# Performance work log

Hardware: AMD Instinct MI355X
Metric: run time of the kernel (lower is better)

The kernel has to match this reference:

```python
import jax, jax.numpy as jnp
import numpy as np

N = 100000   # nodes
E = 1600000  # edges
F_IN = 32    # num_features
H = 16       # hidden_size (hardcoded as conv2 input in source)
C = 10       # num_classes
K = 2        # kernel_size (dim=1)


def setup_inputs() -> dict:
    key = jax.random.key(0)
    ks = jax.random.split(key, 9)
    x = jax.random.normal(ks[0], (N, F_IN), dtype=jnp.float32)
    edge_index = jax.random.randint(ks[1], (2, E), 0, N, dtype=jnp.int64)
    edge_attr = jax.random.uniform(ks[2], (E, 1), dtype=jnp.float32)
    s1 = 1.0 / np.sqrt(F_IN)
    s2 = 1.0 / np.sqrt(H)
    W1 = jax.random.normal(ks[3], (K, F_IN, H), dtype=jnp.float32) * s1
    root1 = jax.random.normal(ks[4], (F_IN, H), dtype=jnp.float32) * s1
    b1 = jnp.zeros((H,), dtype=jnp.float32)
    W2 = jax.random.normal(ks[5], (K, H, C), dtype=jnp.float32) * s2
    root2 = jax.random.normal(ks[6], (H, C), dtype=jnp.float32) * s2
    b2 = jnp.zeros((C,), dtype=jnp.float32)
    return {"x": x, "edge_index": edge_index, "edge_attr": edge_attr,
            "W1": W1, "root1": root1, "b1": b1,
            "W2": W2, "root2": root2, "b2": b2}


def spline_conv(x, edge_index, edge_attr, W, root, bias, num_nodes):
    # Open B-spline, degree 1: hat-function basis over K knots.
    k = W.shape[0]
    src, dst = edge_index[0], edge_index[1]
    v = edge_attr[:, 0] * (k - 1)                                   # [E]
    grid = jnp.arange(k, dtype=v.dtype)
    basis = jnp.maximum(0.0, 1.0 - jnp.abs(v[:, None] - grid[None, :]))  # [E,K]
    xe = x[src]                                                      # [E,in] gather
    msg = jnp.einsum('ei,kio,ek->eo', xe, W, basis)                  # per-edge message
    agg = jax.ops.segment_sum(msg, dst, num_segments=num_nodes)      # scatter-add
    deg = jax.ops.segment_sum(jnp.ones((msg.shape[0],), x.dtype), dst,
                              num_segments=num_nodes)
    agg = agg / jnp.maximum(deg, 1.0)[:, None]                       # mean aggregation
    return agg + x @ root + bias


def reference(x, edge_index, edge_attr, W1, root1, b1, W2, root2, b2):
    # Inference mode: F.dropout(training=False) is identity.
    h = jax.nn.elu(spline_conv(x, edge_index, edge_attr, W1, root1, b1, N))
    out = spline_conv(h, edge_index, edge_attr, W2, root2, b2, N)
    return jax.nn.log_softmax(out, axis=1)
```

## Files before the change

### kernel.cpp

```cpp
#include <hip/hip_runtime.h>
#include <math.h>

#define N_NODES 100000
#define E_EDGES 1600000
#define F_IN 32
#define HID 16
#define NC 10
#define SRC_BITS 17
#define SRC_MASK ((1u << SRC_BITS) - 1u)
#define VQ_SCALE 32767.0f
#define CBITS 8
#define BUCKET_N 256
#define NCB ((N_NODES + BUCKET_N - 1) / BUCKET_N)
#define BLK_E 4096
#define NBLK ((E_EDGES + BLK_E - 1) / BLK_E)
#define L1_BLOCKS ((N_NODES + 511) / 512)
#define CAP 6144

__device__ __forceinline__ unsigned int bf16pair(float lo, float hi) {
    unsigned int ulo = __float_as_uint(lo), uhi = __float_as_uint(hi);
    ulo += 0x7fffu + ((ulo >> 16) & 1u);
    uhi += 0x7fffu + ((uhi >> 16) & 1u);
    return (ulo >> 16) | (uhi & 0xffff0000u);
}

__device__ __forceinline__ float lerp_pair(unsigned int pair, float v) {
    float a = __uint_as_float(pair << 16);
    float b = __uint_as_float(pair & 0xffff0000u);
    return fmaf(v, b - a, a);
}

__global__ __launch_bounds__(512) void fused_l1bucket(
    const float* __restrict__ x, const float* __restrict__ W1,
    const float* __restrict__ root1, const float* __restrict__ b1,
    const int* __restrict__ ei, const float* __restrict__ ea,
    unsigned int* __restrict__ y, float* __restrict__ r1,
    int* __restrict__ gcur, int2* __restrict__ ebuf)
{
    if (blockIdx.x >= L1_BLOCKS) {
        __shared__ int h[NCB], base[NCB], cur[NCB];
        int t = threadIdx.x;
        int b = blockIdx.x - L1_BLOCKS;
        for (int i = t; i < NCB; i += 512) { h[i] = 0; cur[i] = 0; }
        __syncthreads();

        const int* dstp = ei + E_EDGES;
        int e0 = b * BLK_E + t * 8;
        int4 dA, dB, sA, sB;
        float4 aA, aB;
        bool fullA = (e0 + 3 < E_EDGES), fullB = (e0 + 7 < E_EDGES);
        if (fullA) {
            dA = *(const int4*)(dstp + e0);
            sA = *(const int4*)(ei + e0);
            aA = *(const float4*)(ea + e0);
            atomicAdd(&h[dA.x >> CBITS], 1);
            atomicAdd(&h[dA.y >> CBITS], 1);
            atomicAdd(&h[dA.z >> CBITS], 1);
            atomicAdd(&h[dA.w >> CBITS], 1);
        }
        if (fullB) {
            dB = *(const int4*)(dstp + e0 + 4);
            sB = *(const int4*)(ei + e0 + 4);
            aB = *(const float4*)(ea + e0 + 4);
            atomicAdd(&h[dB.x >> CBITS], 1);
            atomicAdd(&h[dB.y >> CBITS], 1);
            atomicAdd(&h[dB.z >> CBITS], 1);
            atomicAdd(&h[dB.w >> CBITS], 1);
        }
        if (!fullA || !fullB) {
            int lo = fullA ? e0 + 4 : e0;
            for (int e = lo; e < E_EDGES && e < e0 + 8; e++)
                atomicAdd(&h[dstp[e] >> CBITS], 1);
        }
        __syncthreads();

        for (int s = t; s < NCB; s += 512)
            if (h[s] > 0) base[s] = atomicAdd(&gcur[s], h[s]);
        __syncthreads();

        if (fullA) {
            {
                int s = dA.x >> CBITS;
                int idx = base[s] + atomicAdd(&cur[s], 1);
                unsigned int vq = (unsigned int)(aA.x * VQ_SCALE + 0.5f);
                if (idx < CAP)
                    ebuf[(size_t)s * CAP + idx] = make_int2(dA.x & (BUCKET_N - 1),
                        (int)((vq << SRC_BITS) | (unsigned int)sA.x));
            }
            {
                int s = dA.y >> CBITS;
                int idx = base[s] + atomicAdd(&cur[s], 1);
                unsigned int vq = (unsigned int)(aA.y * VQ_SCALE + 0.5f);
                if (idx < CAP)
                    ebuf[(size_t)s * CAP + idx] = make_int2(dA.y & (BUCKET_N - 1),
                        (int)((vq << SRC_BITS) | (unsigned int)sA.y));
            }
            {
                int s = dA.z >> CBITS;
                int idx = base[s] + atomicAdd(&cur[s], 1);
                unsigned int vq = (unsigned int)(aA.z * VQ_SCALE + 0.5f);
                if (idx < CAP)
                    ebuf[(size_t)s * CAP + idx] = make_int2(dA.z & (BUCKET_N - 1),
                        (int)((vq << SRC_BITS) | (unsigned int)sA.z));
            }
            {
                int s = dA.w >> CBITS;
                int idx = base[s] + atomicAdd(&cur[s], 1);
                unsigned int vq = (unsigned int)(aA.w * VQ_SCALE + 0.5f);
                if (idx < CAP)
                    ebuf[(size_t)s * CAP + idx] = make_int2(dA.w & (BUCKET_N - 1),
                        (int)((vq << SRC_BITS) | (unsigned int)sA.w));
            }
        }
        if (fullB) {
            {
                int s = dB.x >> CBITS;
                int idx = base[s] + atomicAdd(&cur[s], 1);
                unsigned int vq = (unsigned int)(aB.x * VQ_SCALE + 0.5f);
                if (idx < CAP)
                    ebuf[(size_t)s * CAP + idx] = make_int2(dB.x & (BUCKET_N - 1),
                        (int)((vq << SRC_BITS) | (unsigned int)sB.x));
            }
            {
                int s = dB.y >> CBITS;
                int idx = base[s] + atomicAdd(&cur[s], 1);
                unsigned int vq = (unsigned int)(aB.y * VQ_SCALE + 0.5f);
                if (idx < CAP)
                    ebuf[(size_t)s * CAP + idx] = make_int2(dB.y & (BUCKET_N - 1),
                        (int)((vq << SRC_BITS) | (unsigned int)sB.y));
            }
            {
                int s = dB.z >> CBITS;
                int idx = base[s] + atomicAdd(&cur[s], 1);
                unsigned int vq = (unsigned int)(aB.z * VQ_SCALE + 0.5f);
                if (idx < CAP)
                    ebuf[(size_t)s * CAP + idx] = make_int2(dB.z & (BUCKET_N - 1),
                        (int)((vq << SRC_BITS) | (unsigned int)sB.z));
            }
            {
                int s = dB.w >> CBITS;
                int idx = base[s] + atomicAdd(&cur[s], 1);
                unsigned int vq = (unsigned int)(aB.w * VQ_SCALE + 0.5f);
                if (idx < CAP)
                    ebuf[(size_t)s * CAP + idx] = make_int2(dB.w & (BUCKET_N - 1),
                        (int)((vq << SRC_BITS) | (unsigned int)sB.w));
            }
        }
        if (!fullA || !fullB) {
            int lo = fullA ? e0 + 4 : e0;
            for (int e = lo; e < E_EDGES && e < e0 + 8; e++) {
                int dst = dstp[e];
                int s = dst >> CBITS;
                int idx = base[s] + atomicAdd(&cur[s], 1);
                unsigned int vq = (unsigned int)(ea[e] * VQ_SCALE + 0.5f);
                if (idx < CAP)
                    ebuf[(size_t)s * CAP + idx] = make_int2(dst & (BUCKET_N - 1),
                        (int)((vq << SRC_BITS) | (unsigned int)ei[e]));
            }
        }
        return;
    }
    __shared__ float sW0[F_IN * HID], sW1[F_IN * HID], sR[F_IN * HID], sB[HID];
    for (int i = threadIdx.x; i < F_IN * HID; i += 512) {
        sW0[i] = W1[i];
        sW1[i] = W1[F_IN * HID + i];
        sR[i]  = root1[i];
    }
    if (threadIdx.x < HID) sB[threadIdx.x] = b1[threadIdx.x];
    __syncthreads();

    int n = blockIdx.x * 512 + threadIdx.x;
    if (n >= N_NODES) return;

    float xr[F_IN];
    const float4* xp = (const float4*)(x + (size_t)n * F_IN);
    #pragma unroll
    for (int i = 0; i < F_IN / 4; i++) {
        float4 t4 = xp[i];
        xr[i*4+0] = t4.x; xr[i*4+1] = t4.y; xr[i*4+2] = t4.z; xr[i*4+3] = t4.w;
    }

    float a0[HID], a1[HID], ar[HID];
    #pragma unroll
    for (int o = 0; o < HID; o++) { a0[o] = 0.f; a1[o] = 0.f; ar[o] = sB[o]; }
    for (int i = 0; i < F_IN; i++) {
        float xi = xr[i];
        #pragma unroll
        for (int o = 0; o < HID; o++) {
            a0[o] += xi * sW0[i * HID + o];
            a1[o] += xi * sW1[i * HID + o];
            ar[o] += xi * sR[i * HID + o];
        }
    }
    unsigned int* py = y + (size_t)n * 16;
    float* pr = r1 + (size_t)n * HID;
    #pragma unroll
    for (int o = 0; o < HID; o++) {
        py[o] = bf16pair(a0[o], a1[o]);
        pr[o] = ar[o];
    }
}

__global__ __launch_bounds__(1024) void k_bsort(
    const int2* __restrict__ ebuf, const int* __restrict__ gcur,
    unsigned int* __restrict__ es, int* __restrict__ start)
{
    __shared__ int hist[BUCKET_N];
    __shared__ int cursor[BUCKET_N];
    __shared__ int pre[NCB];
    __shared__ int wsum[16], woff[16];
    __shared__ int wsum2[4], woff2[4];
    int t = threadIdx.x;
    int b = blockIdx.x;
    int w = t >> 6, l = t & 63;

    int v = (t < NCB) ? min(gcur[t], CAP) : 0;
    int incl = v;
    #pragma unroll
    for (int off = 1; off < 64; off <<= 1) {
        int u = __shfl_up(incl, off, 64);
        if (l >= off) incl += u;
    }
    if (l == 63) wsum[w] = incl;
    if (t < BUCKET_N) { hist[t] = 0; cursor[t] = 0; }
    __syncthreads();
    if (t == 0) {
        int a = 0;
        #pragma unroll
        for (int i = 0; i < 16; i++) { woff[i] = a; a += wsum[i]; }
    }
    __syncthreads();
    if (t < NCB) pre[t] = woff[w] + incl - v;
    __syncthreads();

    int fill = min(gcur[b], CAP);
    int obase = pre[b];
    const int2* win = ebuf + (size_t)b * CAP;

    for (int j = t; j < fill; j += 1024)
        atomicAdd(&hist[win[j].x], 1);
    __syncthreads();

    int c = (t < BUCKET_N) ? hist[t] : 0;
    int incl2 = c;
    #pragma unroll
    for (int off = 1; off < 64; off <<= 1) {
        int u = __shfl_up(incl2, off, 64);
        if (l >= off) incl2 += u;
    }
    if (w < 4 && l == 63) wsum2[w] = incl2;
    __syncthreads();
    if (t == 0) {
        int acc = 0;
        #pragma unroll
        for (int i = 0; i < 4; i++) { woff2[i] = acc; acc += wsum2[i]; }
    }
    __syncthreads();
    if (t < BUCKET_N) {
        int excl = woff2[w] + incl2 - c;
        hist[t] = excl;
        int node = (b << CBITS) + t;
        if (node < N_NODES) start[node] = obase + excl;
    }
    if (b == 0 && t == 0) start[N_NODES] = E_EDGES;
    __syncthreads();

    for (int j = t; j < fill; j += 1024) {
        int2 p = win[j];
        int off = atomicAdd(&cursor[p.x], 1);
        es[obase + hist[p.x] + off] = (unsigned int)p.y;
    }
}

__global__ __launch_bounds__(256) void k_agg1(
    const unsigned int* __restrict__ es, const int* __restrict__ start,
    const unsigned int* __restrict__ y, const float* __restrict__ r1,
    const float* __restrict__ W2, const float* __restrict__ root2,
    const float* __restrict__ b2,
    unsigned int* __restrict__ z, float* __restrict__ r2)
{
    __shared__ float sW0[HID * NC], sW1[HID * NC], sRt[HID * NC], sB2[NC];
    int t = threadIdx.x;
    if (t < HID * NC) { sW0[t] = W2[t]; sW1[t] = W2[HID * NC + t]; sRt[t] = root2[t]; }
    if (t >= HID * NC && t < HID * NC + NC) sB2[t - HID * NC] = b2[t - HID * NC];
    __syncthreads();

    int idx = blockIdx.x * 256 + t;
    int n = idx >> 2, l = idx & 3;
    if (n >= N_NODES) return;
    int j0 = start[n], j1 = start[n + 1];
    const uint4* yrow = (const uint4*)y;
    float acc[4] = {0.f, 0.f, 0.f, 0.f};
    int j = j0;
    for (; j + 3 < j1; j += 4) {
        unsigned int p0 = es[j], p1 = es[j+1], p2 = es[j+2], p3 = es[j+3];
        uint4 q0 = yrow[(size_t)(p0 & SRC_MASK) * 4 + l];
        uint4 q1 = yrow[(size_t)(p1 & SRC_MASK) * 4 + l];
        uint4 q2 = yrow[(size_t)(p2 & SRC_MASK) * 4 + l];
        uint4 q3 = yrow[(size_t)(p3 & SRC_MASK) * 4 + l];
        float v0 = (float)(p0 >> SRC_BITS) * (1.0f / VQ_SCALE);
        float v1 = (float)(p1 >> SRC_BITS) * (1.0f / VQ_SCALE);
        float v2 = (float)(p2 >> SRC_BITS) * (1.0f / VQ_SCALE);
        float v3 = (float)(p3 >> SRC_BITS) * (1.0f / VQ_SCALE);
        acc[0] += lerp_pair(q0.x, v0); acc[1] += lerp_pair(q0.y, v0);
        acc[2] += lerp_pair(q0.z, v0); acc[3] += lerp_pair(q0.w, v0);
        acc[0] += lerp_pair(q1.x, v1); acc[1] += lerp_pair(q1.y, v1);
        acc[2] += lerp_pair(q1.z, v1); acc[3] += lerp_pair(q1.w, v1);
        acc[0] += lerp_pair(q2.x, v2); acc[1] += lerp_pair(q2.y, v2);
        acc[2] += lerp_pair(q2.z, v2); acc[3] += lerp_pair(q2.w, v2);
        acc[0] += lerp_pair(q3.x, v3); acc[1] += lerp_pair(q3.y, v3);
        acc[2] += lerp_pair(q3.z, v3); acc[3] += lerp_pair(q3.w, v3);
    }
    for (; j < j1; j++) {
        unsigned int p = es[j];
        uint4 q = yrow[(size_t)(p & SRC_MASK) * 4 + l];
        float v = (float)(p >> SRC_BITS) * (1.0f / VQ_SCALE);
        acc[0] += lerp_pair(q.x, v); acc[1] += lerp_pair(q.y, v);
        acc[2] += lerp_pair(q.z, v); acc[3] += lerp_pair(q.w, v);
    }
    float inv = 1.0f / fmaxf((float)(j1 - j0), 1.0f);
    float4 rr = *(const float4*)(r1 + (size_t)n * HID + l * 4);
    float hv[4];
    hv[0] = acc[0] * inv + rr.x;
    hv[1] = acc[1] * inv + rr.y;
    hv[2] = acc[2] * inv + rr.z;
    hv[3] = acc[3] * inv + rr.w;
    #pragma unroll
    for (int e = 0; e < 4; e++) hv[e] = hv[e] > 0.0f ? hv[e] : expm1f(hv[e]);

    int cbase = l * 4;
    float a0[4] = {0.f, 0.f, 0.f, 0.f}, a1[4] = {0.f, 0.f, 0.f, 0.f}, ar[4];
    #pragma unroll
    for (int e = 0; e < 4; e++) { int c = cbase + e; ar[e] = (c < NC) ? sB2[c] : 0.f; }
    #pragma unroll
    for (int s = 0; s < 4; s++) {
        #pragma unroll
        for (int e2 = 0; e2 < 4; e2++) {
            float hi = __shfl(hv[e2], s, 4);
            int i = s * 4 + e2;
            #pragma unroll
            for (int e = 0; e < 4; e++) {
                int c = cbase + e;
                if (c < NC) {
                    a0[e] += hi * sW0[i * NC + c];
                    a1[e] += hi * sW1[i * NC + c];
                    ar[e] += hi * sRt[i * NC + c];
                }
            }
        }
    }
    uint4 zo;
    zo.x = (cbase + 0 < NC) ? bf16pair(a0[0], a1[0]) : 0u;
    zo.y = (cbase + 1 < NC) ? bf16pair(a0[1], a1[1]) : 0u;
    zo.z = (cbase + 2 < NC) ? bf16pair(a0[2], a1[2]) : 0u;
    zo.w = (cbase + 3 < NC) ? bf16pair(a0[3], a1[3]) : 0u;
    ((uint4*)z)[(size_t)n * 4 + l] = zo;
    #pragma unroll
    for (int e = 0; e < 4; e++) {
        int c = cbase + e;
        if (c < NC) r2[(size_t)n * NC + c] = ar[e];
    }
}

__global__ __launch_bounds__(256) void k_agg2(
    const unsigned int* __restrict__ es, const int* __restrict__ start,
    const unsigned int* __restrict__ z,
    const float* __restrict__ r2, float* __restrict__ out)
{
    int idx = blockIdx.x * 256 + threadIdx.x;
    int n = idx >> 2, l = idx & 3;
    if (n >= N_NODES) return;
    int j0 = start[n], j1 = start[n + 1];
    const uint4* zrow = (const uint4*)z;
    float acc[4] = {0.f, 0.f, 0.f, 0.f};
    int j = j0;
    for (; j + 3 < j1; j += 4) {
        unsigned int p0 = es[j], p1 = es[j+1], p2 = es[j+2], p3 = es[j+3];
        uint4 q0 = zrow[(size_t)(p0 & SRC_MASK) * 4 + l];
        uint4 q1 = zrow[(size_t)(p1 & SRC_MASK) * 4 + l];
        uint4 q2 = zrow[(size_t)(p2 & SRC_MASK) * 4 + l];
        uint4 q3 = zrow[(size_t)(p3 & SRC_MASK) * 4 + l];
        float v0 = (float)(p0 >> SRC_BITS) * (1.0f / VQ_SCALE);
        float v1 = (float)(p1 >> SRC_BITS) * (1.0f / VQ_SCALE);
        float v2 = (float)(p2 >> SRC_BITS) * (1.0f / VQ_SCALE);
        float v3 = (float)(p3 >> SRC_BITS) * (1.0f / VQ_SCALE);
        acc[0] += lerp_pair(q0.x, v0); acc[1] += lerp_pair(q0.y, v0);
        acc[2] += lerp_pair(q0.z, v0); acc[3] += lerp_pair(q0.w, v0);
        acc[0] += lerp_pair(q1.x, v1); acc[1] += lerp_pair(q1.y, v1);
        acc[2] += lerp_pair(q1.z, v1); acc[3] += lerp_pair(q1.w, v1);
        acc[0] += lerp_pair(q2.x, v2); acc[1] += lerp_pair(q2.y, v2);
        acc[2] += lerp_pair(q2.z, v2); acc[3] += lerp_pair(q2.w, v2);
        acc[0] += lerp_pair(q3.x, v3); acc[1] += lerp_pair(q3.y, v3);
        acc[2] += lerp_pair(q3.z, v3); acc[3] += lerp_pair(q3.w, v3);
    }
    for (; j < j1; j++) {
        unsigned int p = es[j];
        uint4 q = zrow[(size_t)(p & SRC_MASK) * 4 + l];
        float v = (float)(p >> SRC_BITS) * (1.0f / VQ_SCALE);
        acc[0] += lerp_pair(q.x, v); acc[1] += lerp_pair(q.y, v);
        acc[2] += lerp_pair(q.z, v); acc[3] += lerp_pair(q.w, v);
    }
    float inv = 1.0f / fmaxf((float)(j1 - j0), 1.0f);
    int cbase = l * 4;
    float val[4];
    #pragma unroll
    for (int e = 0; e < 4; e++) {
        int c = cbase + e;
        val[e] = (c < NC) ? acc[e] * inv + r2[(size_t)n * NC + c] : -INFINITY;
    }
    float mx = fmaxf(fmaxf(val[0], val[1]), fmaxf(val[2], val[3]));
    mx = fmaxf(mx, __shfl_xor(mx, 1, 4));
    mx = fmaxf(mx, __shfl_xor(mx, 2, 4));
    float ssum = 0.f;
    #pragma unroll
    for (int e = 0; e < 4; e++) {
        int c = cbase + e;
        if (c < NC) ssum += expf(val[e] - mx);
    }
    ssum += __shfl_xor(ssum, 1, 4);
    ssum += __shfl_xor(ssum, 2, 4);
    float lse = logf(ssum);
    #pragma unroll
    for (int e = 0; e < 4; e++) {
        int c = cbase + e;
        if (c < NC) out[(size_t)n * NC + c] = val[e] - mx - lse;
    }
}

extern "C" void kernel_launch(void* const* d_in, const int* in_sizes, int n_in,
                              void* d_out, int out_size, void* d_ws, size_t ws_size,
                              hipStream_t stream) {
    const float* x     = (const float*)d_in[0];
    const int*   ei    = (const int*)d_in[1];
    const float* ea    = (const float*)d_in[2];
    const float* W1    = (const float*)d_in[3];
    const float* root1 = (const float*)d_in[4];
    const float* b1    = (const float*)d_in[5];
    const float* W2    = (const float*)d_in[6];
    const float* root2 = (const float*)d_in[7];
    const float* b2    = (const float*)d_in[8];
    float* out = (float*)d_out;

    char* wsb = (char*)d_ws;
    int2*         ebuf   = (int2*)wsb;
    unsigned int* es     = (unsigned int*)(wsb + (size_t)NCB * CAP * 8);
    unsigned int* y      = es + (size_t)E_EDGES;
    float*        r1     = (float*)(y + (size_t)N_NODES * 16);
    unsigned int* z      = (unsigned int*)(r1 + (size_t)N_NODES * HID);
    float*        r2     = (float*)(z + (size_t)N_NODES * 16);
    int*          start  = (int*)(r2 + (size_t)N_NODES * NC);
    int*          gcur   = start + N_NODES + 1;

    int aggGrid = (N_NODES * 4 + 255) / 256;

    hipMemsetAsync(gcur, 0, (size_t)NCB * sizeof(int), stream);
    fused_l1bucket<<<L1_BLOCKS + NBLK, 512, 0, stream>>>(x, W1, root1, b1, ei, ea,
                                                         y, r1, gcur, ebuf);
    k_bsort<<<NCB, 1024, 0, stream>>>(ebuf, gcur, es, start);
    k_agg1 <<<aggGrid, 256, 0, stream>>>(es, start, y, r1, W2, root2, b2, z, r2);
    k_agg2 <<<aggGrid, 256, 0, stream>>>(es, start, z, r2, out);
}
```

Baseline: 176.1 us.

## Stage bucketed edges in LDS and write them out bucket-contiguously

New measurement: 170.6 us. 3.1% less time.

```diff
diff --git a/kernel.cpp b/kernel.cpp
--- a/kernel.cpp
+++ b/kernel.cpp
@@ -39,6 +39,10 @@
 {
     if (blockIdx.x >= L1_BLOCKS) {
         __shared__ int h[NCB], base[NCB], cur[NCB];
+        __shared__ int wsum[8], woff[8];
+        __shared__ unsigned int  pay_lds[BLK_E];
+        __shared__ unsigned char dl_lds[BLK_E];
+        __shared__ int           gid_lds[BLK_E];
         int t = threadIdx.x;
         int b = blockIdx.x - L1_BLOCKS;
         for (int i = t; i < NCB; i += 512) { h[i] = 0; cur[i] = 0; }
@@ -75,88 +79,64 @@
         __syncthreads();
 
         for (int s = t; s < NCB; s += 512)
-            if (h[s] > 0) base[s] = atomicAdd(&gcur[s], h[s]);
-        __syncthreads();
+            base[s] = (h[s] > 0) ? atomicAdd(&gcur[s], h[s]) : 0;
+        __syncthreads();
+
+        int w = t >> 6, l = t & 63;
+        int v = (t < NCB) ? h[t] : 0;
+        int incl = v;
+        #pragma unroll
+        for (int off = 1; off < 64; off <<= 1) {
+            int u = __shfl_up(incl, off, 64);
+            if (l >= off) incl += u;
+        }
+        if (l == 63) wsum[w] = incl;
+        __syncthreads();
+        if (t == 0) {
+            int a = 0;
+            #pragma unroll
+            for (int i = 0; i < 8; i++) { woff[i] = a; a += wsum[i]; }
+        }
+        __syncthreads();
+        if (t < NCB) h[t] = woff[w] + incl - v;
+        __syncthreads();
+
+        #define STAGE(dv, sv, av) do {                                          \
+            int s_ = (dv) >> CBITS;                                             \
+            int idx_ = atomicAdd(&cur[s_], 1);                                  \
+            int p_ = h[s_] + idx_;                                              \
+            int g_ = base[s_] + idx_;                                           \
+            gid_lds[p_] = (g_ < CAP) ? (s_ * CAP + g_) : -1;                    \
+            unsigned int vq_ = (unsigned int)((av) * VQ_SCALE + 0.5f);          \
+            pay_lds[p_] = (vq_ << SRC_BITS) | (unsigned int)(sv);               \
+            dl_lds[p_] = (unsigned char)((dv) & (BUCKET_N - 1));                \
+        } while (0)
 
         if (fullA) {
-            {
-                int s = dA.x >> CBITS;
-                int idx = base[s] + atomicAdd(&cur[s], 1);
-                unsigned int vq = (unsigned int)(aA.x * VQ_SCALE + 0.5f);
-                if (idx < CAP)
-                    ebuf[(size_t)s * CAP + idx] = make_int2(dA.x & (BUCKET_N - 1),
-                        (int)((vq << SRC_BITS) | (unsigned int)sA.x));
-            }
-            {
-                int s = dA.y >> CBITS;
-                int idx = base[s] + atomicAdd(&cur[s], 1);
-                unsigned int vq = (unsigned int)(aA.y * VQ_SCALE + 0.5f);
-                if (idx < CAP)
-                    ebuf[(size_t)s * CAP + idx] = make_int2(dA.y & (BUCKET_N - 1),
-                        (int)((vq << SRC_BITS) | (unsigned int)sA.y));
-            }
-            {
-                int s = dA.z >> CBITS;
-                int idx = base[s] + atomicAdd(&cur[s], 1);
-                unsigned int vq = (unsigned int)(aA.z * VQ_SCALE + 0.5f);
-                if (idx < CAP)
-                    ebuf[(size_t)s * CAP + idx] = make_int2(dA.z & (BUCKET_N - 1),
-                        (int)((vq << SRC_BITS) | (unsigned int)sA.z));
-            }
-            {
-                int s = dA.w >> CBITS;
-                int idx = base[s] + atomicAdd(&cur[s], 1);
-                unsigned int vq = (unsigned int)(aA.w * VQ_SCALE + 0.5f);
-                if (idx < CAP)
-                    ebuf[(size_t)s * CAP + idx] = make_int2(dA.w & (BUCKET_N - 1),
-                        (int)((vq << SRC_BITS) | (unsigned int)sA.w));
-            }
+            STAGE(dA.x, sA.x, aA.x);
+            STAGE(dA.y, sA.y, aA.y);
+            STAGE(dA.z, sA.z, aA.z);
+            STAGE(dA.w, sA.w, aA.w);
         }
         if (fullB) {
-            {
-                int s = dB.x >> CBITS;
-                int idx = base[s] + atomicAdd(&cur[s], 1);
-                unsigned int vq = (unsigned int)(aB.x * VQ_SCALE + 0.5f);
-                if (idx < CAP)
-                    ebuf[(size_t)s * CAP + idx] = make_int2(dB.x & (BUCKET_N - 1),
-                        (int)((vq << SRC_BITS) | (unsigned int)sB.x));
-            }
-            {
-                int s = dB.y >> CBITS;
-                int idx = base[s] + atomicAdd(&cur[s], 1);
-                unsigned int vq = (unsigned int)(aB.y * VQ_SCALE + 0.5f);
-                if (idx < CAP)
-                    ebuf[(size_t)s * CAP + idx] = make_int2(dB.y & (BUCKET_N - 1),
-                        (int)((vq << SRC_BITS) | (unsigned int)sB.y));
-            }
-            {
-                int s = dB.z >> CBITS;
-                int idx = base[s] + atomicAdd(&cur[s], 1);
-                unsigned int vq = (unsigned int)(aB.z * VQ_SCALE + 0.5f);
-                if (idx < CAP)
-                    ebuf[(size_t)s * CAP + idx] = make_int2(dB.z & (BUCKET_N - 1),
-                        (int)((vq << SRC_BITS) | (unsigned int)sB.z));
-            }
-            {
-                int s = dB.w >> CBITS;
-                int idx = base[s] + atomicAdd(&cur[s], 1);
-                unsigned int vq = (unsigned int)(aB.w * VQ_SCALE + 0.5f);
-                if (idx < CAP)
-                    ebuf[(size_t)s * CAP + idx] = make_int2(dB.w & (BUCKET_N - 1),
-                        (int)((vq << SRC_BITS) | (unsigned int)sB.w));
-            }
+            STAGE(dB.x, sB.x, aB.x);
+            STAGE(dB.y, sB.y, aB.y);
+            STAGE(dB.z, sB.z, aB.z);
+            STAGE(dB.w, sB.w, aB.w);
         }
         if (!fullA || !fullB) {
             int lo = fullA ? e0 + 4 : e0;
-            for (int e = lo; e < E_EDGES && e < e0 + 8; e++) {
-                int dst = dstp[e];
-                int s = dst >> CBITS;
-                int idx = base[s] + atomicAdd(&cur[s], 1);
-                unsigned int vq = (unsigned int)(ea[e] * VQ_SCALE + 0.5f);
-                if (idx < CAP)
-                    ebuf[(size_t)s * CAP + idx] = make_int2(dst & (BUCKET_N - 1),
-                        (int)((vq << SRC_BITS) | (unsigned int)ei[e]));
-            }
+            for (int e = lo; e < E_EDGES && e < e0 + 8; e++)
+                STAGE(dstp[e], ei[e], ea[e]);
+        }
+        #undef STAGE
+        __syncthreads();
+
+        int nE = min(BLK_E, E_EDGES - b * BLK_E);
+        for (int p = t; p < nE; p += 512) {
+            int g = gid_lds[p];
+            if (g >= 0)
+                ebuf[g] = make_int2((int)dl_lds[p], (int)pay_lds[p]);
         }
         return;
     }
```
